# Optimization experiments

Measured on AMD Instinct MI355X. Metric: run time of the kernel, lower is better.

Reference implementation:

```python
import jax, jax.numpy as jnp
import numpy as np

B, S, H = 4, 2048, 1024
D_FF = 4 * H
NUM_EXPERTS = 8
TOP_K = 2


def setup_inputs() -> dict:
    key = jax.random.key(0)
    ks = jax.random.split(key, 6)
    scale = 0.02
    return {
        "hidden_states": jax.random.normal(ks[0], (B, S, H), dtype=jnp.float32),
        "w_router": jax.random.normal(ks[1], (NUM_EXPERTS, H), dtype=jnp.float32) * scale,
        "w1": jax.random.normal(ks[2], (NUM_EXPERTS, D_FF, H), dtype=jnp.float32) * scale,
        "b1": jnp.zeros((NUM_EXPERTS, D_FF), dtype=jnp.float32),
        "w2": jax.random.normal(ks[3], (NUM_EXPERTS, H, D_FF), dtype=jnp.float32) * scale,
        "b2": jnp.zeros((NUM_EXPERTS, H), dtype=jnp.float32),
    }


def reference(hidden_states, w_router, w1, b1, w2, b2):
    Bc, Sc, Hc = hidden_states.shape
    E = w_router.shape[0]
    dtype = hidden_states.dtype

    # Router: logits [B, S, E], top-k, softmax over the k selected logits.
    router_logits = jnp.einsum("bsh,eh->bse", hidden_states, w_router)
    topk_values, topk_indices = jax.lax.top_k(router_logits, TOP_K)
    topk_weights = jax.nn.softmax(topk_values.astype(jnp.float32), axis=-1).astype(dtype)

    # Per-token combine weight for each expert: [B, S, E] -> [T, E].
    # (Equivalent to the torch sort/group + weighted index_add_ combine.)
    combine = jnp.sum(
        jax.nn.one_hot(topk_indices, E, dtype=dtype) * topk_weights[..., None], axis=-2
    )
    flat = hidden_states.reshape(-1, Hc)          # [T, H]
    cw = combine.reshape(-1, E)                    # [T, E]

    # Dense-equivalent MoE: each expert MLP runs on all tokens, scaled by its
    # combine weight (zero for unrouted tokens) -> identical math to gather/scatter.
    mixed = jnp.zeros_like(flat)
    for e in range(E):
        h1 = jax.nn.gelu(flat @ w1[e].T + b1[e], approximate=False)  # [T, 4H]
        mixed = mixed + cw[:, e:e + 1] * (h1 @ w2[e].T + b2[e])
    return mixed.reshape(Bc, Sc, Hc)
```

## Files before the change

### kernel.cpp

```cpp
#include <hip/hip_runtime.h>
#include <hip/hip_bf16.h>
#include <math.h>


#define TT  8192
#define HD  1024
#define DFF 4096
#define NE  8
#define ROWCAP 17408
#define MAXTILES 136

typedef __attribute__((ext_vector_type(8))) short short8;
typedef __attribute__((ext_vector_type(4))) float f32x4;

static __device__ __forceinline__ unsigned short f2bf(float f) {
    unsigned int u = __float_as_uint(f);
    unsigned int r = (u + 0x7fffu + ((u >> 16) & 1u)) >> 16;
    return (unsigned short)r;
}

static __device__ __forceinline__ float bf2f(unsigned short u) {
    return __uint_as_float((unsigned int)u << 16);
}

static __device__ __forceinline__ float gelu_fast(float v) {
    const float s = v * (1.5957691f + 0.07135481f * v * v);
    return v / (1.f + __expf(-s));
}

static __device__ __forceinline__ void gload_lds16(const void* gp, void* lp) {
    __builtin_amdgcn_global_load_lds(
        (__attribute__((address_space(1))) void*)(void*)gp,
        (__attribute__((address_space(3))) void*)lp,
        16, 0, 0);
}

__global__ __launch_bounds__(256) void cvt_w_kernel(const float* __restrict__ s,
                                                    unsigned short* __restrict__ d) {
    const long i = (long)blockIdx.x * 256 + threadIdx.x;
    float4 v = ((const float4*)s)[i];
    ushort4 o;
    o.x = f2bf(v.x); o.y = f2bf(v.y); o.z = f2bf(v.z); o.w = f2bf(v.w);
    ((ushort4*)d)[i] = o;
}

__global__ __launch_bounds__(256) void router_kernel(const float* __restrict__ x,
                                                     const float* __restrict__ wr,
                                                     int* __restrict__ tokE,
                                                     float* __restrict__ tokW,
                                                     int* __restrict__ counts) {
    const int token = blockIdx.x * 4 + (threadIdx.x >> 6);
    const int lane = threadIdx.x & 63;
    const float* xp = x + (long)token * HD;
    double lg[NE];
#pragma unroll
    for (int e = 0; e < NE; ++e) {
        const float* wp = wr + e * HD;
        double s = 0.0;
        for (int i = lane; i < HD; i += 64) s += (double)xp[i] * (double)wp[i];
#pragma unroll
        for (int off = 32; off > 0; off >>= 1) s += __shfl_xor(s, off, 64);
        lg[e] = s;
    }
    if (lane == 0) {
        int i0 = 0; double v0 = lg[0];
#pragma unroll
        for (int e = 1; e < NE; ++e) if (lg[e] > v0) { v0 = lg[e]; i0 = e; }
        int i1 = -1; double v1 = -1e300;
#pragma unroll
        for (int e = 0; e < NE; ++e) if (e != i0 && lg[e] > v1) { v1 = lg[e]; i1 = e; }
        double p = exp(v1 - v0);
        double d = 1.0 + p;
        tokE[token * 2] = i0;     tokW[token * 2] = (float)(1.0 / d);
        tokE[token * 2 + 1] = i1; tokW[token * 2 + 1] = (float)(p / d);
        atomicAdd(&counts[i0], 1);
        atomicAdd(&counts[i1], 1);
    }
}

__global__ __launch_bounds__(256) void init_setup_kernel(const int* __restrict__ counts,
                                                         int* __restrict__ cursor,
                                                         int* __restrict__ tileExpert,
                                                         int* __restrict__ tileRow0,
                                                         int* __restrict__ rowTok) {
    const int i = blockIdx.x * 256 + threadIdx.x;
    if (i < ROWCAP) rowTok[i] = 0;
    if (blockIdx.x == gridDim.x - 1 && threadIdx.x == 0) {
        int off = 0, t = 0;
        for (int e = 0; e < NE; ++e) {
            cursor[e] = off;
            const int padded = (counts[e] + 127) & ~127;
            for (int j = 0; j < padded / 128; ++j) {
                tileExpert[t] = e;
                tileRow0[t] = off + j * 128;
                ++t;
            }
            off += padded;
        }
        for (; t < MAXTILES; ++t) tileExpert[t] = -1;
    }
}

__global__ __launch_bounds__(256) void scatter_kernel(const int* __restrict__ tokE,
                                                      int* __restrict__ cursor,
                                                      int* __restrict__ rowTok,
                                                      int* __restrict__ posOf) {
    const int t = blockIdx.x * 256 + threadIdx.x;
#pragma unroll
    for (int j = 0; j < 2; ++j) {
        const int e = tokE[t * 2 + j];
        const int pos = atomicAdd(&cursor[e], 1);
        rowTok[pos] = t;
        posOf[t * 2 + j] = pos;
    }
}

__global__ __launch_bounds__(256) void gather_kernel(const float* __restrict__ x,
                                                     const int* __restrict__ rowTok,
                                                     unsigned short* __restrict__ Xg) {
    const int row = blockIdx.x;
    const int tok = rowTok[row];
    const float4 v = ((const float4*)(x + (long)tok * HD))[threadIdx.x];
    ushort4 o;
    o.x = f2bf(v.x); o.y = f2bf(v.y); o.z = f2bf(v.z); o.w = f2bf(v.w);
    ((ushort4*)(Xg + (long)row * HD))[threadIdx.x] = o;
}

template <int EPI, int N, int K>
__global__ __launch_bounds__(256) void gemm_moe(
    const unsigned short* __restrict__ A,
    const unsigned short* __restrict__ W,
    const int* __restrict__ tileExpert,
    const int* __restrict__ tileRow0,
    unsigned short* __restrict__ Hout,
    const float* __restrict__ bias) {
    const int e = tileExpert[blockIdx.x];
    if (e < 0) return;

    __shared__ unsigned short As[128 * 32];
    __shared__ unsigned short Bs[128 * 32];

    const int tid = threadIdx.x;
    const int lane = tid & 63;
    const int quad = lane >> 4;
    const int l15 = lane & 15;
    const int wy = (tid >> 6) >> 1;
    const int wx = (tid >> 6) & 1;
    const long row0 = tileRow0[blockIdx.x];
    const long n0 = (long)blockIdx.y * 128;
    const unsigned short* Ab = A + row0 * K;
    const unsigned short* Bb = W + ((long)e * N + n0) * K;

    f32x4 acc[4][4];
#pragma unroll
    for (int i = 0; i < 4; ++i)
#pragma unroll
        for (int j = 0; j < 4; ++j) acc[i][j] = (f32x4){0.f, 0.f, 0.f, 0.f};

    for (int k0 = 0; k0 < K; k0 += 32) {
#pragma unroll
        for (int it = 0; it < 2; ++it) {
            const int c = it * 256 + tid;
            gload_lds16(Ab + (long)(c >> 2) * K + k0 + (c & 3) * 8, As + c * 8);
            gload_lds16(Bb + (long)(c >> 2) * K + k0 + (c & 3) * 8, Bs + c * 8);
        }
        __syncthreads();

        short8 af[4];
#pragma unroll
        for (int mi = 0; mi < 4; ++mi)
            af[mi] = *(const short8*)(As + (wy * 64 + mi * 16 + l15) * 32 + quad * 8);
#pragma unroll
        for (int ni = 0; ni < 4; ++ni) {
            const short8 bf = *(const short8*)(Bs + (wx * 64 + ni * 16 + l15) * 32 + quad * 8);
#pragma unroll
            for (int mi = 0; mi < 4; ++mi)
                acc[mi][ni] = __builtin_amdgcn_mfma_f32_16x16x32_bf16(
                    af[mi], bf, acc[mi][ni], 0, 0, 0);
        }
        __syncthreads();
    }

#pragma unroll
    for (int mi = 0; mi < 4; ++mi) {
        const int lrow0 = wy * 64 + mi * 16 + quad * 4;
#pragma unroll
        for (int ni = 0; ni < 4; ++ni) {
            const long col = n0 + wx * 64 + ni * 16 + l15;
            const float bcol = bias[(long)e * N + col];
#pragma unroll
            for (int r = 0; r < 4; ++r) {
                const long grow = row0 + lrow0 + r;
                float v = acc[mi][ni][r] + bcol;
                if constexpr (EPI == 0) v = gelu_fast(v);
                Hout[grow * N + col] = f2bf(v);
            }
        }
    }
}

__global__ __launch_bounds__(256) void combine_kernel(const unsigned short* __restrict__ Y,
                                                      const int* __restrict__ posOf,
                                                      const float* __restrict__ tokW,
                                                      float* __restrict__ out) {
    const int t = blockIdx.x;
    const int p0 = posOf[t * 2];
    const int p1 = posOf[t * 2 + 1];
    const float w0 = tokW[t * 2];
    const float w1 = tokW[t * 2 + 1];
    const ushort4 a = ((const ushort4*)(Y + (long)p0 * HD))[threadIdx.x];
    const ushort4 b = ((const ushort4*)(Y + (long)p1 * HD))[threadIdx.x];
    float4 o;
    o.x = w0 * bf2f(a.x) + w1 * bf2f(b.x);
    o.y = w0 * bf2f(a.y) + w1 * bf2f(b.y);
    o.z = w0 * bf2f(a.z) + w1 * bf2f(b.z);
    o.w = w0 * bf2f(a.w) + w1 * bf2f(b.w);
    ((float4*)(out + (long)t * HD))[threadIdx.x] = o;
}

extern "C" void kernel_launch(void* const* d_in, const int* in_sizes, int n_in,
                              void* d_out, int out_size, void* d_ws, size_t ws_size,
                              hipStream_t stream) {
    const float* x  = (const float*)d_in[0];
    const float* wr = (const float*)d_in[1];
    const float* w1 = (const float*)d_in[2];
    const float* b1 = (const float*)d_in[3];
    const float* w2 = (const float*)d_in[4];
    const float* b2 = (const float*)d_in[5];
    float* out = (float*)d_out;

    char* p = (char*)d_ws;
    auto alloc = [&](size_t bytes) {
        char* r = p;
        p += (bytes + 255) & ~(size_t)255;
        return r;
    };
    unsigned short* Xg  = (unsigned short*)alloc((size_t)ROWCAP * HD * 2);
    unsigned short* H1g = (unsigned short*)alloc((size_t)ROWCAP * DFF * 2);
    unsigned short* Wb  = (unsigned short*)alloc((size_t)NE * DFF * HD * 2);
    int*   rowTok  = (int*)alloc((size_t)ROWCAP * 4);
    int*   posOf   = (int*)alloc((size_t)TT * 2 * 4);
    int*   tokE    = (int*)alloc((size_t)TT * 2 * 4);
    float* tokW    = (float*)alloc((size_t)TT * 2 * 4);
    int*   counts  = (int*)alloc(64);
    int*   cursor  = (int*)alloc(64);
    int*   tileExpert = (int*)alloc(MAXTILES * 4);
    int*   tileRow0   = (int*)alloc(MAXTILES * 4);

    unsigned short* Yg = Xg;

    hipMemsetAsync(counts, 0, 64, stream);

    router_kernel<<<dim3(TT / 4), dim3(256), 0, stream>>>(x, wr, tokE, tokW, counts);
    init_setup_kernel<<<dim3(ROWCAP / 256 + 1), dim3(256), 0, stream>>>(
        counts, cursor, tileExpert, tileRow0, rowTok);
    scatter_kernel<<<dim3(TT / 256), dim3(256), 0, stream>>>(tokE, cursor, rowTok, posOf);
    gather_kernel<<<dim3(ROWCAP), dim3(256), 0, stream>>>(x, rowTok, Xg);

    cvt_w_kernel<<<dim3(NE * DFF * HD / 4 / 256), dim3(256), 0, stream>>>(w1, Wb);
    gemm_moe<0, DFF, HD><<<dim3(MAXTILES, DFF / 128), dim3(256), 0, stream>>>(
        Xg, Wb, tileExpert, tileRow0, H1g, b1);

    cvt_w_kernel<<<dim3(NE * HD * DFF / 4 / 256), dim3(256), 0, stream>>>(w2, Wb);
    gemm_moe<1, HD, DFF><<<dim3(MAXTILES, HD / 128), dim3(256), 0, stream>>>(
        H1g, Wb, tileExpert, tileRow0, Yg, b2);

    combine_kernel<<<dim3(TT), dim3(256), 0, stream>>>(Yg, posOf, tokW, out);
}
```

Baseline: 1.091 ms.

## Replace MoE GEMMs with 256-row, 512-thread pipelined MFMA kernel and fuse weight conversion

Swaps the 128x128 single-buffered grouped GEMM for a 256xBN tile kernel with 8 waves. It double-buffers LDS with XOR swizzle, interleaves quarter-tile loads with MFMA under explicit barriers and setprio, and remaps workgroups across XCDs. Routing pads each expert to 256 rows, and both weight matrices are converted to bf16 in one grid-stride launch when the workspace is large enough. The router now stages the routing weights in LDS and computes all expert logits in one pass. This targets low MFMA utilisation and global load latency, at the cost of more padding waste, more registers and LDS per block, and an extra weight buffer.

```diff
diff --git a/kernel.cpp b/kernel.cpp
--- a/kernel.cpp
+++ b/kernel.cpp
@@ -7,8 +7,8 @@
 #define HD  1024
 #define DFF 4096
 #define NE  8
-#define ROWCAP 17408
-#define MAXTILES 136
+#define ROWCAP 18432
+#define MAXT 72
 
 typedef __attribute__((ext_vector_type(8))) short short8;
 typedef __attribute__((ext_vector_type(4))) float f32x4;
@@ -35,13 +35,42 @@
         16, 0, 0);
 }
 
+#define BARM                                        \
+    __builtin_amdgcn_s_barrier();                   \
+    asm volatile("" ::: "memory");                  \
+    __builtin_amdgcn_sched_barrier(0)
+#define LGKM0                                       \
+    asm volatile("s_waitcnt lgkmcnt(0)" ::: "memory"); \
+    __builtin_amdgcn_sched_barrier(0)
+#define PRIO1 __builtin_amdgcn_s_setprio(1)
+#define PRIO0 __builtin_amdgcn_s_setprio(0)
+
+__global__ __launch_bounds__(256) void cvt_w2_kernel(const float* __restrict__ s1,
+                                                     unsigned short* __restrict__ d1,
+                                                     const float* __restrict__ s2,
+                                                     unsigned short* __restrict__ d2,
+                                                     long n4) {
+    for (long i = (long)blockIdx.x * 256 + threadIdx.x; i < 2 * n4;
+         i += (long)gridDim.x * 256) {
+        const bool second = i >= n4;
+        const long j = second ? i - n4 : i;
+        float4 v = second ? ((const float4*)s2)[j] : ((const float4*)s1)[j];
+        ushort4 o;
+        o.x = f2bf(v.x); o.y = f2bf(v.y); o.z = f2bf(v.z); o.w = f2bf(v.w);
+        if (second) ((ushort4*)d2)[j] = o; else ((ushort4*)d1)[j] = o;
+    }
+}
+
 __global__ __launch_bounds__(256) void cvt_w_kernel(const float* __restrict__ s,
-                                                    unsigned short* __restrict__ d) {
-    const long i = (long)blockIdx.x * 256 + threadIdx.x;
-    float4 v = ((const float4*)s)[i];
-    ushort4 o;
-    o.x = f2bf(v.x); o.y = f2bf(v.y); o.z = f2bf(v.z); o.w = f2bf(v.w);
-    ((ushort4*)d)[i] = o;
+                                                    unsigned short* __restrict__ d,
+                                                    long n4) {
+    for (long i = (long)blockIdx.x * 256 + threadIdx.x; i < n4;
+         i += (long)gridDim.x * 256) {
+        float4 v = ((const float4*)s)[i];
+        ushort4 o;
+        o.x = f2bf(v.x); o.y = f2bf(v.y); o.z = f2bf(v.z); o.w = f2bf(v.w);
+        ((ushort4*)d)[i] = o;
+    }
 }
 
 __global__ __launch_bounds__(256) void router_kernel(const float* __restrict__ x,
@@ -49,15 +78,27 @@
                                                      int* __restrict__ tokE,
                                                      float* __restrict__ tokW,
                                                      int* __restrict__ counts) {
-    const int token = blockIdx.x * 4 + (threadIdx.x >> 6);
-    const int lane = threadIdx.x & 63;
+    __shared__ float wrs[NE * HD];
+    const int tid = threadIdx.x;
+#pragma unroll
+    for (int i = 0; i < NE * HD / 4 / 256; ++i)
+        ((float4*)wrs)[i * 256 + tid] = ((const float4*)wr)[i * 256 + tid];
+    __syncthreads();
+
+    const int token = blockIdx.x * 4 + (tid >> 6);
+    const int lane = tid & 63;
     const float* xp = x + (long)token * HD;
     double lg[NE];
 #pragma unroll
+    for (int e = 0; e < NE; ++e) lg[e] = 0.0;
+    for (int i = lane; i < HD; i += 64) {
+        const double xv = (double)xp[i];
+#pragma unroll
+        for (int e = 0; e < NE; ++e) lg[e] += xv * (double)wrs[e * HD + i];
+    }
+#pragma unroll
     for (int e = 0; e < NE; ++e) {
-        const float* wp = wr + e * HD;
-        double s = 0.0;
-        for (int i = lane; i < HD; i += 64) s += (double)xp[i] * (double)wp[i];
+        double s = lg[e];
 #pragma unroll
         for (int off = 32; off > 0; off >>= 1) s += __shfl_xor(s, off, 64);
         lg[e] = s;
@@ -80,8 +121,8 @@
 
 __global__ __launch_bounds__(256) void init_setup_kernel(const int* __restrict__ counts,
                                                          int* __restrict__ cursor,
-                                                         int* __restrict__ tileExpert,
-                                                         int* __restrict__ tileRow0,
+                                                         int* __restrict__ tE,
+                                                         int* __restrict__ tR,
                                                          int* __restrict__ rowTok) {
     const int i = blockIdx.x * 256 + threadIdx.x;
     if (i < ROWCAP) rowTok[i] = 0;
@@ -89,15 +130,13 @@
         int off = 0, t = 0;
         for (int e = 0; e < NE; ++e) {
             cursor[e] = off;
-            const int padded = (counts[e] + 127) & ~127;
-            for (int j = 0; j < padded / 128; ++j) {
-                tileExpert[t] = e;
-                tileRow0[t] = off + j * 128;
-                ++t;
+            const int padded = (counts[e] + 255) & ~255;
+            for (int j = 0; j < padded / 256; ++j) {
+                tE[t] = e; tR[t] = off + j * 256; ++t;
             }
             off += padded;
         }
-        for (; t < MAXTILES; ++t) tileExpert[t] = -1;
+        for (; t < MAXT; ++t) tE[t] = -1;
     }
 }
 
@@ -126,77 +165,189 @@
     ((ushort4*)(Xg + (long)row * HD))[threadIdx.x] = o;
 }
 
-template <int EPI, int N, int K>
-__global__ __launch_bounds__(256) void gemm_moe(
+template <int EPI, int N, int K, int BN>
+__global__ __launch_bounds__(512, 2) void gemm4p(
     const unsigned short* __restrict__ A,
     const unsigned short* __restrict__ W,
-    const int* __restrict__ tileExpert,
-    const int* __restrict__ tileRow0,
+    const int* __restrict__ tE,
+    const int* __restrict__ tR,
     unsigned short* __restrict__ Hout,
     const float* __restrict__ bias) {
-    const int e = tileExpert[blockIdx.x];
+    constexpr int BM = 256, BK = 64, NT = K / BK;
+    constexpr int NREP = BN / 64;
+    constexpr int NREP2 = NREP / 2;
+    constexpr int NB = BN / 64;
+    constexpr int NB2 = NB / 2;
+    constexpr int HB = BN / 8;
+    constexpr int LOG2HB = (BN == 256) ? 5 : 4;
+    constexpr int VB = NB2 + 2;
+    constexpr int AHALF = BM * BK;
+    constexpr int HALF = (BM + BN) * BK;
+
+    const int nwg = gridDim.x * gridDim.y;
+    int bid = blockIdx.y * gridDim.x + blockIdx.x;
+    bid = (bid & 7) * (nwg >> 3) + (bid >> 3);
+    const int tix = bid % gridDim.x;
+    const int niy = bid / gridDim.x;
+
+    const int e = tE[tix];
     if (e < 0) return;
 
-    __shared__ unsigned short As[128 * 32];
-    __shared__ unsigned short Bs[128 * 32];
+    __shared__ unsigned short smem[2 * HALF];
 
     const int tid = threadIdx.x;
     const int lane = tid & 63;
     const int quad = lane >> 4;
     const int l15 = lane & 15;
-    const int wy = (tid >> 6) >> 1;
-    const int wx = (tid >> 6) & 1;
-    const long row0 = tileRow0[blockIdx.x];
-    const long n0 = (long)blockIdx.y * 128;
+    const int wid = tid >> 6;
+    const int wrr = wid >> 2;
+    const int wcc = wid & 3;
+
+    const long row0 = tR[tix];
+    const long n0 = (long)niy * BN;
     const unsigned short* Ab = A + row0 * K;
     const unsigned short* Bb = W + ((long)e * N + n0) * K;
 
-    f32x4 acc[4][4];
-#pragma unroll
-    for (int i = 0; i < 4; ++i)
-#pragma unroll
-        for (int j = 0; j < 4; ++j) acc[i][j] = (f32x4){0.f, 0.f, 0.f, 0.f};
-
-    for (int k0 = 0; k0 < K; k0 += 32) {
-#pragma unroll
-        for (int it = 0; it < 2; ++it) {
-            const int c = it * 256 + tid;
-            gload_lds16(Ab + (long)(c >> 2) * K + k0 + (c & 3) * 8, As + c * 8);
-            gload_lds16(Bb + (long)(c >> 2) * K + k0 + (c & 3) * 8, Bs + c * 8);
-        }
-        __syncthreads();
-
-        short8 af[4];
-#pragma unroll
-        for (int mi = 0; mi < 4; ++mi)
-            af[mi] = *(const short8*)(As + (wy * 64 + mi * 16 + l15) * 32 + quad * 8);
-#pragma unroll
-        for (int ni = 0; ni < 4; ++ni) {
-            const short8 bf = *(const short8*)(Bs + (wx * 64 + ni * 16 + l15) * 32 + quad * 8);
-#pragma unroll
-            for (int mi = 0; mi < 4; ++mi)
-                acc[mi][ni] = __builtin_amdgcn_mfma_f32_16x16x32_bf16(
-                    af[mi], bf, acc[mi][ni], 0, 0, 0);
-        }
-        __syncthreads();
-    }
-
-#pragma unroll
-    for (int mi = 0; mi < 4; ++mi) {
-        const int lrow0 = wy * 64 + mi * 16 + quad * 4;
-#pragma unroll
-        for (int ni = 0; ni < 4; ++ni) {
-            const long col = n0 + wx * 64 + ni * 16 + l15;
+    const unsigned short* aS[4];
+    int aD[4];
+#pragma unroll
+    for (int i = 0; i < 4; ++i) {
+        const int c = i * 512 + tid;
+        const int r = c >> 3, s = c & 7;
+        aS[i] = Ab + (long)r * K + (s ^ (r & 7)) * 8;
+        aD[i] = c * 8;
+    }
+    const unsigned short* bS[NB];
+    int bD[NB];
+#pragma unroll
+    for (int i = 0; i < NB; ++i) {
+        const int c = i * 512 + tid;
+        const int rho = c >> 3, s = c & 7;
+        const int rl = rho & (BN / 2 - 1);
+        const int r = (rl & (HB - 1)) + ((rl >> LOG2HB) << (LOG2HB + 1)) +
+                      ((rho >= BN / 2) ? HB : 0);
+        bS[i] = Bb + (long)r * K + (s ^ (rho & 7)) * 8;
+        bD[i] = c * 8;
+    }
+
+    auto stgA = [&](int buf, int t, int g) {
+        unsigned short* dst = smem + buf * HALF;
+        gload_lds16(aS[g] + (long)t * BK, dst + aD[g]);
+        gload_lds16(aS[g + 2] + (long)t * BK, dst + aD[g + 2]);
+    };
+    auto stgB = [&](int buf, int t, int g) {
+        unsigned short* dst = smem + buf * HALF + AHALF;
+#pragma unroll
+        for (int j = 0; j < NB2; ++j)
+            gload_lds16(bS[g * NB2 + j] + (long)t * BK, dst + bD[g * NB2 + j]);
+    };
+    auto rdA = [&](const unsigned short* Ac, int mi, int ks) -> short8 {
+        const int row = wrr * 128 + mi * 16 + l15;
+        return *(const short8*)(Ac + row * BK + ((ks * 4 + quad) ^ (row & 7)) * 8);
+    };
+    auto rdB = [&](const unsigned short* Bc, int ni, int ks) -> short8 {
+        int rho;
+        if constexpr (BN == 256)
+            rho = (ni & 1) * 16 + l15 + wcc * 32 + ((ni & 2) ? 128 : 0);
+        else
+            rho = l15 + wcc * 16 + ni * 64;
+        return *(const short8*)(Bc + rho * BK + ((ks * 4 + quad) ^ (rho & 7)) * 8);
+    };
+
+#define RD_A(AF, AC, HM)                                                \
+    _Pragma("unroll") for (int i_ = 0; i_ < 4; ++i_)                    \
+    _Pragma("unroll") for (int k_ = 0; k_ < 2; ++k_)                    \
+        AF[i_][k_] = rdA(AC, (HM) * 4 + i_, k_);
+#define RD_B(BF, BC, HN)                                                \
+    _Pragma("unroll") for (int j_ = 0; j_ < NREP2; ++j_)                \
+    _Pragma("unroll") for (int k_ = 0; k_ < 2; ++k_)                    \
+        BF[j_][k_] = rdB(BC, (HN) * NREP2 + j_, k_);
+#define MMA_Q(AF, BF, HM, HN)                                           \
+    _Pragma("unroll") for (int i_ = 0; i_ < 4; ++i_)                    \
+    _Pragma("unroll") for (int j_ = 0; j_ < NREP2; ++j_)                \
+    _Pragma("unroll") for (int k_ = 0; k_ < 2; ++k_)                    \
+        acc[(HM) * 4 + i_][(HN) * NREP2 + j_] =                         \
+            __builtin_amdgcn_mfma_f32_16x16x32_bf16(                    \
+                AF[i_][k_], BF[j_][k_],                                 \
+                acc[(HM) * 4 + i_][(HN) * NREP2 + j_], 0, 0, 0);
+#define VMC(NN) asm volatile("s_waitcnt vmcnt(%0)" ::"n"(NN) : "memory")
+
+    f32x4 acc[8][NREP];
+#pragma unroll
+    for (int i = 0; i < 8; ++i)
+#pragma unroll
+        for (int j = 0; j < NREP; ++j) acc[i][j] = (f32x4){0.f, 0.f, 0.f, 0.f};
+
+    stgA(0, 0, 0); stgB(0, 0, 0); stgA(0, 0, 1); stgB(0, 0, 1);
+    VMC(VB);
+    BARM;
+
+#pragma unroll 1
+    for (int t = 0; t < NT - 1; ++t) {
+        const int cur = t & 1;
+        const int nb = cur ^ 1;
+        const unsigned short* Ac = smem + cur * HALF;
+        const unsigned short* Bc = Ac + AHALF;
+        short8 af0[4][2], af1[4][2], bf0[NREP2][2], bf1[NREP2][2];
+        RD_A(af0, Ac, 0); RD_B(bf0, Bc, 0);
+        stgA(nb, t + 1, 0);
+        BARM; LGKM0;
+        PRIO1; MMA_Q(af0, bf0, 0, 0); PRIO0;
+        VMC(VB); BARM;
+        RD_A(af1, Ac, 1);
+        stgB(nb, t + 1, 0);
+        BARM; LGKM0;
+        PRIO1; MMA_Q(af1, bf0, 1, 0); PRIO0;
+        VMC(VB); BARM;
+        RD_B(bf1, Bc, 1);
+        stgA(nb, t + 1, 1);
+        BARM; LGKM0;
+        PRIO1; MMA_Q(af1, bf1, 1, 1); PRIO0;
+        BARM;
+        stgB(nb, t + 1, 1);
+        BARM;
+        PRIO1; MMA_Q(af0, bf1, 0, 1); PRIO0;
+        VMC(VB); BARM;
+    }
+
+    {
+        const int cur = (NT - 1) & 1;
+        const unsigned short* Ac = smem + cur * HALF;
+        const unsigned short* Bc = Ac + AHALF;
+        short8 af0[4][2], af1[4][2], bf0[NREP2][2], bf1[NREP2][2];
+        RD_A(af0, Ac, 0); RD_B(bf0, Bc, 0);
+        BARM; LGKM0;
+        PRIO1; MMA_Q(af0, bf0, 0, 0); PRIO0;
+        VMC(NB2); BARM;
+        RD_A(af1, Ac, 1);
+        BARM; LGKM0;
+        PRIO1; MMA_Q(af1, bf0, 1, 0); PRIO0;
+        VMC(0); BARM;
+        RD_B(bf1, Bc, 1);
+        BARM; LGKM0;
+        PRIO1; MMA_Q(af1, bf1, 1, 1); PRIO0;
+        PRIO1; MMA_Q(af0, bf1, 0, 1); PRIO0;
+    }
+
+#pragma unroll
+    for (int mi = 0; mi < 8; ++mi) {
+        const long grow0 = row0 + wrr * 128 + mi * 16 + quad * 4;
+#pragma unroll
+        for (int ni = 0; ni < NREP; ++ni) {
+            const long col = n0 + wcc * (BN / 4) + ni * 16 + l15;
             const float bcol = bias[(long)e * N + col];
 #pragma unroll
             for (int r = 0; r < 4; ++r) {
-                const long grow = row0 + lrow0 + r;
                 float v = acc[mi][ni][r] + bcol;
                 if constexpr (EPI == 0) v = gelu_fast(v);
-                Hout[grow * N + col] = f2bf(v);
+                Hout[(grow0 + r) * N + col] = f2bf(v);
             }
         }
     }
+#undef RD_A
+#undef RD_B
+#undef MMA_Q
+#undef VMC
 }
 
 __global__ __launch_bounds__(256) void combine_kernel(const unsigned short* __restrict__ Y,
@@ -229,6 +380,9 @@
     const float* b2 = (const float*)d_in[5];
     float* out = (float*)d_out;
 
+    const size_t WBYTES = (size_t)NE * DFF * HD * 2;
+    const bool full = ws_size >= (size_t)326 * 1024 * 1024;
+
     char* p = (char*)d_ws;
     auto alloc = [&](size_t bytes) {
         char* r = p;
@@ -237,33 +391,41 @@
     };
     unsigned short* Xg  = (unsigned short*)alloc((size_t)ROWCAP * HD * 2);
     unsigned short* H1g = (unsigned short*)alloc((size_t)ROWCAP * DFF * 2);
-    unsigned short* Wb  = (unsigned short*)alloc((size_t)NE * DFF * HD * 2);
+    unsigned short* Wb1 = (unsigned short*)alloc(WBYTES);
+    unsigned short* Wb2 = full ? (unsigned short*)alloc(WBYTES) : Wb1;
     int*   rowTok  = (int*)alloc((size_t)ROWCAP * 4);
     int*   posOf   = (int*)alloc((size_t)TT * 2 * 4);
     int*   tokE    = (int*)alloc((size_t)TT * 2 * 4);
     float* tokW    = (float*)alloc((size_t)TT * 2 * 4);
     int*   counts  = (int*)alloc(64);
     int*   cursor  = (int*)alloc(64);
-    int*   tileExpert = (int*)alloc(MAXTILES * 4);
-    int*   tileRow0   = (int*)alloc(MAXTILES * 4);
+    int*   tE      = (int*)alloc(MAXT * 4);
+    int*   tR      = (int*)alloc(MAXT * 4);
 
     unsigned short* Yg = Xg;
 
     hipMemsetAsync(counts, 0, 64, stream);
+
+    const long n4w = (long)NE * DFF * HD / 4;
+    if (full) {
+        cvt_w2_kernel<<<dim3(8192), dim3(256), 0, stream>>>(w1, Wb1, w2, Wb2, n4w);
+    } else {
+        cvt_w_kernel<<<dim3(4096), dim3(256), 0, stream>>>(w1, Wb1, n4w);
+    }
 
     router_kernel<<<dim3(TT / 4), dim3(256), 0, stream>>>(x, wr, tokE, tokW, counts);
     init_setup_kernel<<<dim3(ROWCAP / 256 + 1), dim3(256), 0, stream>>>(
-        counts, cursor, tileExpert, tileRow0, rowTok);
+        counts, cursor, tE, tR, rowTok);
     scatter_kernel<<<dim3(TT / 256), dim3(256), 0, stream>>>(tokE, cursor, rowTok, posOf);
     gather_kernel<<<dim3(ROWCAP), dim3(256), 0, stream>>>(x, rowTok, Xg);
 
-    cvt_w_kernel<<<dim3(NE * DFF * HD / 4 / 256), dim3(256), 0, stream>>>(w1, Wb);
-    gemm_moe<0, DFF, HD><<<dim3(MAXTILES, DFF / 128), dim3(256), 0, stream>>>(
-        Xg, Wb, tileExpert, tileRow0, H1g, b1);
-
-    cvt_w_kernel<<<dim3(NE * HD * DFF / 4 / 256), dim3(256), 0, stream>>>(w2, Wb);
-    gemm_moe<1, HD, DFF><<<dim3(MAXTILES, HD / 128), dim3(256), 0, stream>>>(
-        H1g, Wb, tileExpert, tileRow0, Yg, b2);
+    gemm4p<0, DFF, HD, 256><<<dim3(MAXT, DFF / 256), dim3(512), 0, stream>>>(
+        Xg, Wb1, tE, tR, H1g, b1);
+
+    if (!full)
+        cvt_w_kernel<<<dim3(4096), dim3(256), 0, stream>>>(w2, Wb1, n4w);
+    gemm4p<1, HD, DFF, 128><<<dim3(MAXT, HD / 128), dim3(512), 0, stream>>>(
+        H1g, Wb2, tE, tR, Yg, b2);
 
     combine_kernel<<<dim3(TT), dim3(256), 0, stream>>>(Yg, posOf, tokW, out);
 }
```

After: 1.015 ms. 7.0% less time.
